# Kernel tuning notes

Hardware: AMD Instinct MI355X
Metric: run time of the kernel (lower is better)

The kernel has to match this reference:

```python
import jax, jax.numpy as jnp
import numpy as np

B, T, I, H, O = 256, 512, 64, 256, 16
THRESH = 1.0

def _xavier(key, fan_out, fan_in):
    bound = float(np.sqrt(6.0 / (fan_in + fan_out)))
    return jax.random.uniform(key, (fan_out, fan_in), jnp.float32, -bound, bound)

def setup_inputs() -> dict:
    key = jax.random.key(0)
    k = jax.random.split(key, 4)
    return {
        "x": jax.random.normal(k[0], (B, T, I), jnp.float32),
        "W_i2h": _xavier(k[1], H, I),
        "b_i2h": jnp.zeros((H,), jnp.float32),
        "W_h2h": 0.001 * jax.random.normal(k[2], (H, H), jnp.float32),  # trunc_normal std=0.001 approx
        "b_h2h": jnp.zeros((H,), jnp.float32),
        "W_out": _xavier(k[3], O, H),
        "b_out": jnp.zeros((O,), jnp.float32),
        "hidden_init": jnp.zeros((1, H), jnp.float32),
    }

def reference(x, W_i2h, b_i2h, W_h2h, b_h2h, W_out, b_out, hidden_init):
    # Precompute input projection for all timesteps in one GEMM: [B,T,H]
    xi = jnp.einsum('bti,hi->bth', x, W_i2h) + b_i2h
    h0 = jnp.tile(hidden_init, (x.shape[0], 1))  # [B,H]

    def step(h, xt):
        pre = h + xt + h @ W_h2h.T + b_h2h
        a = jnp.minimum(jax.nn.relu(pre), jnp.float32(THRESH))
        return a, a

    hidden, rnn_out_t = jax.lax.scan(step, h0, jnp.swapaxes(xi, 0, 1))  # [T,B,H]
    rnn_out = jnp.swapaxes(rnn_out_t, 0, 1)  # [B,T,H]
    output = rnn_out @ W_out.T + b_out  # [B,T,O]
    return (output, hidden, rnn_out)
```

## Files before the change

kernel.cpp:

```cpp
#include <hip/hip_runtime.h>

#define NB 256
#define NT 512
#define NI 64
#define NH 256
#define NO 16

typedef __attribute__((ext_vector_type(8))) short short8;
typedef __attribute__((ext_vector_type(8))) __bf16 bf16x8;
typedef __attribute__((ext_vector_type(2))) float f32x2;
typedef __attribute__((ext_vector_type(4))) float f32x4;
typedef __attribute__((ext_vector_type(4))) int int4v;
typedef __attribute__((ext_vector_type(8))) int int8v;

#define XI_STRIDE 260

__device__ __forceinline__ unsigned short f2bf(float f) {
  unsigned u = __builtin_bit_cast(unsigned, f);
  u += 0x7fffu + ((u >> 16) & 1u);
  return (unsigned short)(u >> 16);
}

__device__ __forceinline__ f32x4 mfma16(short8 a, short8 b, f32x4 c) {
  return __builtin_amdgcn_mfma_f32_16x16x32_bf16(
      __builtin_bit_cast(bf16x8, a), __builtin_bit_cast(bf16x8, b), c, 0, 0, 0);
}

__device__ __forceinline__ f32x4 mfma_fp8(int8v a, int8v b, f32x4 c) {
  return __builtin_amdgcn_mfma_scale_f32_16x16x128_f8f6f4(
      a, b, c, 0, 0, 0, 0x7f7f7f7f, 0, 0x7f7f7f7f);
}

__device__ __forceinline__ short8 pack8v(f32x4 lo, f32x4 hi) {
  short8 r;
#pragma unroll
  for (int i = 0; i < 4; ++i) {
    r[i]     = (short)f2bf(lo[i]);
    r[i + 4] = (short)f2bf(hi[i]);
  }
  return r;
}

__device__ __forceinline__ short8 pack8(const float* __restrict__ p) {
  return pack8v(*reinterpret_cast<const f32x4*>(p),
                *reinterpret_cast<const f32x4*>(p + 4));
}

__device__ __forceinline__ void step_barrier() {
  asm volatile("s_waitcnt lgkmcnt(0)" ::: "memory");
  __builtin_amdgcn_s_barrier();
  asm volatile("" ::: "memory");
}

__global__ __launch_bounds__(512, 2)
void rnn_fused(const float* __restrict__ x,  const float* __restrict__ Wi,
               const float* __restrict__ bi, const float* __restrict__ Wh,
               const float* __restrict__ bh, const float* __restrict__ Wo,
               const float* __restrict__ bo, const float* __restrict__ h0,
               float* __restrict__ dout)
{
  const int b   = blockIdx.x;
  const int tid = threadIdx.x;
  const int w   = tid >> 6;
  const int l   = tid & 63;
  const int lg  = l >> 4;
  const int ll  = l & 15;

  __shared__ __align__(16) unsigned char  hq8[2][256];
  __shared__ __align__(16) unsigned short rnnwin[16 * NH];
  __shared__ __align__(16) float          xi_t[16 * XI_STRIDE];

  float* outp = dout;
  float* hidp = dout + (size_t)NB * NT * NO;
  float* rnnp = hidp + (size_t)NB * NH;

  const f32x4 cz = {0.f, 0.f, 0.f, 0.f};

  int8v wq8[2][2];
  float dq[2];
#pragma unroll
  for (int jt = 0; jt < 2; ++jt) {
    const int j = w * 32 + 2 * ll + jt;
    const float* wr = Wh + (size_t)j * NH;
    float m = 0.f;
#pragma unroll
    for (int kc = 0; kc < 2; ++kc)
#pragma unroll
      for (int q8 = 0; q8 < 8; ++q8) {
        f32x4 v = *reinterpret_cast<const f32x4*>(wr + kc * 128 + lg * 32 + q8 * 4);
#pragma unroll
        for (int i = 0; i < 4; ++i) m = fmaxf(m, fabsf(v[i]));
      }
    m = fmaxf(m, __shfl_xor(m, 16));
    m = fmaxf(m, __shfl_xor(m, 32));
    const float s = (m > 0.f) ? 224.f / m : 0.f;
    dq[jt] = m * (1.f / 224.f);
#pragma unroll
    for (int kc = 0; kc < 2; ++kc) {
      int8v t8;
#pragma unroll
      for (int q8 = 0; q8 < 8; ++q8) {
        f32x4 v = *reinterpret_cast<const f32x4*>(wr + kc * 128 + lg * 32 + q8 * 4);
        int lo = __builtin_amdgcn_cvt_pk_fp8_f32(v[0] * s, v[1] * s, 0, false);
        t8[q8] = __builtin_amdgcn_cvt_pk_fp8_f32(v[2] * s, v[3] * s, lo, true);
      }
      wq8[jt][kc] = t8;
    }
  }

  short8 wif[2][2];
#pragma unroll
  for (int jt = 0; jt < 2; ++jt) {
    const int j = w * 32 + jt * 16 + ll;
#pragma unroll
    for (int kx = 0; kx < 2; ++kx)
      wif[jt][kx] = pack8(Wi + (size_t)j * NI + kx * 32 + lg * 8);
  }

  const int je = w * 32 + 2 * ll;
  const float breg0 = bi[je]     + bh[je];
  const float breg1 = bi[je + 1] + bh[je + 1];
  const float bout = bo[ll];

  float h_reg0 = h0[je];
  float h_reg1 = h0[je + 1];

  if (tid < 128) {
    int v = __builtin_amdgcn_cvt_pk_fp8_f32(h0[2 * tid], h0[2 * tid + 1], 0, false);
    *(unsigned short*)&hq8[0][2 * tid] = (unsigned short)v;
  }

  const float* xrow = x + (size_t)b * NT * NI + (size_t)ll * NI + lg * 8;
  f32x4 xpre[4];
  xpre[0] = *reinterpret_cast<const f32x4*>(xrow);
  xpre[1] = *reinterpret_cast<const f32x4*>(xrow + 4);
  xpre[2] = *reinterpret_cast<const f32x4*>(xrow + 32);
  xpre[3] = *reinterpret_cast<const f32x4*>(xrow + 36);

  __syncthreads();

  auto outproj = [&](int tbase) {
    f32x4 oacc = cz;
#pragma unroll
    for (int kt = 0; kt < 8; ++kt) {
      short8 wo = pack8(Wo + (size_t)ll * NH + kt * 32 + lg * 8);
      const char* ap = (const char*)rnnwin + ll * 512 +
                       ((kt * 64 + lg * 16) ^ (ll << 4));
      short8 af = *reinterpret_cast<const short8*>(ap);
      oacc = mfma16(af, wo, oacc);
    }
#pragma unroll
    for (int r = 0; r < 4; ++r) {
      const int tp = lg * 4 + r;
      outp[((size_t)b * NT + tbase - 16 + tp) * NO + ll] = oacc[r] + bout;
    }
  };

#pragma unroll 1
  for (int t0 = 0; t0 < NT; t0 += 16) {
    if (t0 > 0 && w == 0) outproj(t0);
    {
      short8 xf0 = pack8v(xpre[0], xpre[1]);
      short8 xf1 = pack8v(xpre[2], xpre[3]);
#pragma unroll
      for (int jt = 0; jt < 2; ++jt) {
        f32x4 acc = mfma16(xf0, wif[jt][0], cz);
        acc = mfma16(xf1, wif[jt][1], acc);
        const int j = w * 32 + jt * 16 + ll;
#pragma unroll
        for (int r = 0; r < 4; ++r)
          xi_t[(lg * 4 + r) * XI_STRIDE + j] = acc[r];
      }
    }
    if (t0 + 16 < NT) {
      const float* xp = x + (size_t)b * NT * NI + (size_t)(t0 + 16 + ll) * NI + lg * 8;
      xpre[0] = *reinterpret_cast<const f32x4*>(xp);
      xpre[1] = *reinterpret_cast<const f32x4*>(xp + 4);
      xpre[2] = *reinterpret_cast<const f32x4*>(xp + 32);
      xpre[3] = *reinterpret_cast<const f32x4*>(xp + 36);
    }
    step_barrier();

#define STEP(TT)                                                               \
    {                                                                          \
      const int t    = (TT);                                                   \
      const int trow = t & 15;                                                 \
      const int p    = t & 1;                                                  \
      const unsigned char* hb = hq8[p];                                        \
      int8v A0, A1;                                                            \
      *(int4v*)&A0       = *(const int4v*)(hb + lg * 32);                      \
      *((int4v*)&A0 + 1) = *(const int4v*)(hb + lg * 32 + 16);                 \
      *(int4v*)&A1       = *(const int4v*)(hb + 128 + lg * 32);                \
      *((int4v*)&A1 + 1) = *(const int4v*)(hb + 128 + lg * 32 + 16);           \
      f32x2 xi2 = *(const f32x2*)&xi_t[trow * XI_STRIDE + je];                 \
      const float hxi0 = h_reg0 + xi2[0] + breg0;                              \
      const float hxi1 = h_reg1 + xi2[1] + breg1;                              \
      f32x4 acc0 = mfma_fp8(A0, wq8[0][0], cz);                                \
      f32x4 acc1 = mfma_fp8(A0, wq8[1][0], cz);                                \
      acc0 = mfma_fp8(A1, wq8[0][1], acc0);                                    \
      acc1 = mfma_fp8(A1, wq8[1][1], acc1);                                    \
      const float a0 = fminf(fmaxf(fmaf(acc0[0], dq[0], hxi0), 0.f), 1.f);     \
      const float a1 = fminf(fmaxf(fmaf(acc1[0], dq[1], hxi1), 0.f), 1.f);     \
      h_reg0 = a0; h_reg1 = a1;                                                \
      if (lg == 0) {                                                           \
        int hv = __builtin_amdgcn_cvt_pk_fp8_f32(a0, a1, 0, false);            \
        *(unsigned short*)&hq8[p ^ 1][je] = (unsigned short)hv;                \
        *(unsigned*)((char*)rnnwin + trow * 512 +                              \
                     ((4 * (w * 16 + ll)) ^ (trow << 4))) =                    \
            (unsigned)f2bf(a0) | ((unsigned)f2bf(a1) << 16);                   \
        f32x2 o2; o2[0] = a0; o2[1] = a1;                                      \
        *(f32x2*)(rnnp + ((size_t)b * NT + t) * NH + je) = o2;                 \
      }                                                                        \
      step_barrier();                                                          \
    }

#pragma unroll 1
    for (int tt = 0; tt < 16; tt += 2) {
      STEP(t0 + tt)
      STEP(t0 + tt + 1)
    }
#undef STEP
  }

  if (w == 0) outproj(NT);
  if (lg == 0) {
    f32x2 h2; h2[0] = h_reg0; h2[1] = h_reg1;
    *(f32x2*)(hidp + (size_t)b * NH + je) = h2;
  }
}

extern "C" void kernel_launch(void* const* d_in, const int* in_sizes, int n_in,
                              void* d_out, int out_size, void* d_ws, size_t ws_size,
                              hipStream_t stream) {
  const float* x  = (const float*)d_in[0];
  const float* Wi = (const float*)d_in[1];
  const float* bi = (const float*)d_in[2];
  const float* Wh = (const float*)d_in[3];
  const float* bh = (const float*)d_in[4];
  const float* Wo = (const float*)d_in[5];
  const float* bo = (const float*)d_in[6];
  const float* h0 = (const float*)d_in[7];
  rnn_fused<<<dim3(NB), dim3(512), 0, stream>>>(x, Wi, bi, Wh, bh, Wo, bo, h0,
                                                (float*)d_out);
}
```

Before: 206.0 us.

## Split recurrence across 16 waves, one hidden unit per lane

Doubles the block to 1024 threads so each wave owns 16 hidden units and runs two fp8 MFMAs per step instead of four. This shortens the serial per-step critical path. The input projection, with the bias folded in, is stored per hidden unit so each lane loads its 16 timesteps into registers once per window. The output-projection duty rotates across waves. In exchange, each step's barrier now synchronises twice as many waves, and register pressure per thread rises under the new launch bounds.

```diff
diff --git a/kernel.cpp b/kernel.cpp
--- a/kernel.cpp
+++ b/kernel.cpp
@@ -8,12 +8,9 @@
 
 typedef __attribute__((ext_vector_type(8))) short short8;
 typedef __attribute__((ext_vector_type(8))) __bf16 bf16x8;
-typedef __attribute__((ext_vector_type(2))) float f32x2;
 typedef __attribute__((ext_vector_type(4))) float f32x4;
 typedef __attribute__((ext_vector_type(4))) int int4v;
 typedef __attribute__((ext_vector_type(8))) int int8v;
-
-#define XI_STRIDE 260
 
 __device__ __forceinline__ unsigned short f2bf(float f) {
   unsigned u = __builtin_bit_cast(unsigned, f);
@@ -52,7 +49,7 @@
   asm volatile("" ::: "memory");
 }
 
-__global__ __launch_bounds__(512, 2)
+__global__ __launch_bounds__(1024, 4)
 void rnn_fused(const float* __restrict__ x,  const float* __restrict__ Wi,
                const float* __restrict__ bi, const float* __restrict__ Wh,
                const float* __restrict__ bh, const float* __restrict__ Wo,
@@ -68,7 +65,7 @@
 
   __shared__ __align__(16) unsigned char  hq8[2][256];
   __shared__ __align__(16) unsigned short rnnwin[16 * NH];
-  __shared__ __align__(16) float          xi_t[16 * XI_STRIDE];
+  __shared__ __align__(16) float          xi_lds[NH * 20];
 
   float* outp = dout;
   float* hidp = dout + (size_t)NB * NT * NO;
@@ -76,11 +73,12 @@
 
   const f32x4 cz = {0.f, 0.f, 0.f, 0.f};
 
-  int8v wq8[2][2];
-  float dq[2];
-#pragma unroll
-  for (int jt = 0; jt < 2; ++jt) {
-    const int j = w * 32 + 2 * ll + jt;
+  const int j   = w * 16 + ll;
+  const int j20 = j * 20;
+
+  int8v wq8[2];
+  float dq;
+  {
     const float* wr = Wh + (size_t)j * NH;
     float m = 0.f;
 #pragma unroll
@@ -94,7 +92,7 @@
     m = fmaxf(m, __shfl_xor(m, 16));
     m = fmaxf(m, __shfl_xor(m, 32));
     const float s = (m > 0.f) ? 224.f / m : 0.f;
-    dq[jt] = m * (1.f / 224.f);
+    dq = m * (1.f / 224.f);
 #pragma unroll
     for (int kc = 0; kc < 2; ++kc) {
       int8v t8;
@@ -104,26 +102,18 @@
         int lo = __builtin_amdgcn_cvt_pk_fp8_f32(v[0] * s, v[1] * s, 0, false);
         t8[q8] = __builtin_amdgcn_cvt_pk_fp8_f32(v[2] * s, v[3] * s, lo, true);
       }
-      wq8[jt][kc] = t8;
-    }
-  }
-
-  short8 wif[2][2];
-#pragma unroll
-  for (int jt = 0; jt < 2; ++jt) {
-    const int j = w * 32 + jt * 16 + ll;
-#pragma unroll
-    for (int kx = 0; kx < 2; ++kx)
-      wif[jt][kx] = pack8(Wi + (size_t)j * NI + kx * 32 + lg * 8);
-  }
-
-  const int je = w * 32 + 2 * ll;
-  const float breg0 = bi[je]     + bh[je];
-  const float breg1 = bi[je + 1] + bh[je + 1];
+      wq8[kc] = t8;
+    }
+  }
+
+  short8 wif[2];
+#pragma unroll
+  for (int kx = 0; kx < 2; ++kx)
+    wif[kx] = pack8(Wi + (size_t)j * NI + kx * 32 + lg * 8);
+
+  const float breg = bi[j] + bh[j];
   const float bout = bo[ll];
-
-  float h_reg0 = h0[je];
-  float h_reg1 = h0[je + 1];
+  float h_reg = h0[j];
 
   if (tid < 128) {
     int v = __builtin_amdgcn_cvt_pk_fp8_f32(h0[2 * tid], h0[2 * tid + 1], 0, false);
@@ -156,21 +146,46 @@
     }
   };
 
+#define STEP(TT, XIV)                                                          \
+  {                                                                            \
+    const int t    = (TT);                                                     \
+    const int trow = t & 15;                                                   \
+    const int p    = t & 1;                                                    \
+    const unsigned char* hb = hq8[p];                                          \
+    int8v A0, A1;                                                              \
+    *(int4v*)&A0       = *(const int4v*)(hb + lg * 32);                        \
+    *((int4v*)&A0 + 1) = *(const int4v*)(hb + lg * 32 + 16);                   \
+    *(int4v*)&A1       = *(const int4v*)(hb + 128 + lg * 32);                  \
+    *((int4v*)&A1 + 1) = *(const int4v*)(hb + 128 + lg * 32 + 16);             \
+    const float hx = h_reg + (XIV);                   \
+    f32x4 acc0 = mfma_fp8(A0, wq8[0], cz);                                     \
+    f32x4 acc1 = mfma_fp8(A1, wq8[1], cz);                                     \
+    const float a = fminf(fmaxf(fmaf(acc0[0] + acc1[0], dq, hx), 0.f), 1.f);   \
+    h_reg = a;                                                                 \
+    if (lg == 0) {                                                             \
+      int hv = __builtin_amdgcn_cvt_pk_fp8_f32(a, a, 0, false);                \
+      hq8[p ^ 1][j] = (unsigned char)hv;                                       \
+      unsigned bfp;                                                            \
+      asm("v_cvt_pk_bf16_f32 %0, %1, %2" : "=v"(bfp) : "v"(a), "v"(a));        \
+      *(unsigned short*)((char*)rnnwin + trow * 512 +                          \
+                         ((2 * j) ^ (trow << 4))) = (unsigned short)bfp;       \
+      rnnp[((size_t)b * NT + t) * NH + j] = a;                                 \
+    }                                                                          \
+    step_barrier();                                                            \
+  }
+
 #pragma unroll 1
   for (int t0 = 0; t0 < NT; t0 += 16) {
-    if (t0 > 0 && w == 0) outproj(t0);
+    if (t0 > 0 && w == (((t0 >> 4) - 1) & 15)) outproj(t0);
     {
       short8 xf0 = pack8v(xpre[0], xpre[1]);
       short8 xf1 = pack8v(xpre[2], xpre[3]);
-#pragma unroll
-      for (int jt = 0; jt < 2; ++jt) {
-        f32x4 acc = mfma16(xf0, wif[jt][0], cz);
-        acc = mfma16(xf1, wif[jt][1], acc);
-        const int j = w * 32 + jt * 16 + ll;
-#pragma unroll
-        for (int r = 0; r < 4; ++r)
-          xi_t[(lg * 4 + r) * XI_STRIDE + j] = acc[r];
-      }
+      f32x4 acc = mfma16(xf0, wif[0], cz);
+      acc = mfma16(xf1, wif[1], acc);
+      f32x4 xo;
+#pragma unroll
+      for (int r = 0; r < 4; ++r) xo[r] = acc[r] + breg;
+      *(f32x4*)&xi_lds[j20 + lg * 4] = xo;
     }
     if (t0 + 16 < NT) {
       const float* xp = x + (size_t)b * NT * NI + (size_t)(t0 + 16 + ll) * NI + lg * 8;
@@ -181,52 +196,24 @@
     }
     step_barrier();
 
-#define STEP(TT)                                                               \
-    {                                                                          \
-      const int t    = (TT);                                                   \
-      const int trow = t & 15;                                                 \
-      const int p    = t & 1;                                                  \
-      const unsigned char* hb = hq8[p];                                        \
-      int8v A0, A1;                                                            \
-      *(int4v*)&A0       = *(const int4v*)(hb + lg * 32);                      \
-      *((int4v*)&A0 + 1) = *(const int4v*)(hb + lg * 32 + 16);                 \
-      *(int4v*)&A1       = *(const int4v*)(hb + 128 + lg * 32);                \
-      *((int4v*)&A1 + 1) = *(const int4v*)(hb + 128 + lg * 32 + 16);           \
-      f32x2 xi2 = *(const f32x2*)&xi_t[trow * XI_STRIDE + je];                 \
-      const float hxi0 = h_reg0 + xi2[0] + breg0;                              \
-      const float hxi1 = h_reg1 + xi2[1] + breg1;                              \
-      f32x4 acc0 = mfma_fp8(A0, wq8[0][0], cz);                                \
-      f32x4 acc1 = mfma_fp8(A0, wq8[1][0], cz);                                \
-      acc0 = mfma_fp8(A1, wq8[0][1], acc0);                                    \
-      acc1 = mfma_fp8(A1, wq8[1][1], acc1);                                    \
-      const float a0 = fminf(fmaxf(fmaf(acc0[0], dq[0], hxi0), 0.f), 1.f);     \
-      const float a1 = fminf(fmaxf(fmaf(acc1[0], dq[1], hxi1), 0.f), 1.f);     \
-      h_reg0 = a0; h_reg1 = a1;                                                \
-      if (lg == 0) {                                                           \
-        int hv = __builtin_amdgcn_cvt_pk_fp8_f32(a0, a1, 0, false);            \
-        *(unsigned short*)&hq8[p ^ 1][je] = (unsigned short)hv;                \
-        *(unsigned*)((char*)rnnwin + trow * 512 +                              \
-                     ((4 * (w * 16 + ll)) ^ (trow << 4))) =                    \
-            (unsigned)f2bf(a0) | ((unsigned)f2bf(a1) << 16);                   \
-        f32x2 o2; o2[0] = a0; o2[1] = a1;                                      \
-        *(f32x2*)(rnnp + ((size_t)b * NT + t) * NH + je) = o2;                 \
-      }                                                                        \
-      step_barrier();                                                          \
-    }
-
-#pragma unroll 1
-    for (int tt = 0; tt < 16; tt += 2) {
-      STEP(t0 + tt)
-      STEP(t0 + tt + 1)
-    }
+    f32x4 xq0 = *(const f32x4*)&xi_lds[j20];
+    f32x4 xq1 = *(const f32x4*)&xi_lds[j20 + 4];
+    f32x4 xq2 = *(const f32x4*)&xi_lds[j20 + 8];
+    f32x4 xq3 = *(const f32x4*)&xi_lds[j20 + 12];
+
+    STEP(t0 + 0,  xq0[0]) STEP(t0 + 1,  xq0[1])
+    STEP(t0 + 2,  xq0[2]) STEP(t0 + 3,  xq0[3])
+    STEP(t0 + 4,  xq1[0]) STEP(t0 + 5,  xq1[1])
+    STEP(t0 + 6,  xq1[2]) STEP(t0 + 7,  xq1[3])
+    STEP(t0 + 8,  xq2[0]) STEP(t0 + 9,  xq2[1])
+    STEP(t0 + 10, xq2[2]) STEP(t0 + 11, xq2[3])
+    STEP(t0 + 12, xq3[0]) STEP(t0 + 13, xq3[1])
+    STEP(t0 + 14, xq3[2]) STEP(t0 + 15, xq3[3])
+  }
 #undef STEP
-  }
-
-  if (w == 0) outproj(NT);
-  if (lg == 0) {
-    f32x2 h2; h2[0] = h_reg0; h2[1] = h_reg1;
-    *(f32x2*)(hidp + (size_t)b * NH + je) = h2;
-  }
+
+  if (w == 15) outproj(NT);
+  if (lg == 0) hidp[(size_t)b * NH + j] = h_reg;
 }
 
 extern "C" void kernel_launch(void* const* d_in, const int* in_sizes, int n_in,
@@ -240,6 +227,6 @@
   const float* Wo = (const float*)d_in[5];
   const float* bo = (const float*)d_in[6];
   const float* h0 = (const float*)d_in[7];
-  rnn_fused<<<dim3(NB), dim3(512), 0, stream>>>(x, Wi, bi, Wh, bh, Wo, bo, h0,
-                                                (float*)d_out);
-}
+  rnn_fused<<<dim3(NB), dim3(1024), 0, stream>>>(x, Wi, bi, Wh, bh, Wo, bo, h0,
+                                                 (float*)d_out);
+}
```

Measured after the change: 249.7 us. 21.2% more time.

## Prefetch xi into registers per chunk, split MFMA chains, rotate outproj wave

Applied to the files above, without the earlier changes.

The xi tile is stored transposed (hidden-major) with the bias folded in. Each thread loads its 16 timesteps of xi into registers once per 16-step chunk, so the per-step LDS read and bias add leave the serial recurrence. The two dependent fp8 MFMAs per output become four independent MFMAs summed afterwards, and the clamp uses med3, both to shorten the per-step latency chain. The output-projection work now rotates across waves instead of always landing on wave 0, at the cost of more registers from full unrolling.

```diff
diff --git a/kernel.cpp b/kernel.cpp
--- a/kernel.cpp
+++ b/kernel.cpp
@@ -12,8 +12,6 @@
 typedef __attribute__((ext_vector_type(4))) float f32x4;
 typedef __attribute__((ext_vector_type(4))) int int4v;
 typedef __attribute__((ext_vector_type(8))) int int8v;
-
-#define XI_STRIDE 260
 
 __device__ __forceinline__ unsigned short f2bf(float f) {
   unsigned u = __builtin_bit_cast(unsigned, f);
@@ -68,7 +66,7 @@
 
   __shared__ __align__(16) unsigned char  hq8[2][256];
   __shared__ __align__(16) unsigned short rnnwin[16 * NH];
-  __shared__ __align__(16) float          xi_t[16 * XI_STRIDE];
+  __shared__ __align__(16) float          xi_t[NH * 20];
 
   float* outp = dout;
   float* hidp = dout + (size_t)NB * NT * NO;
@@ -109,17 +107,17 @@
   }
 
   short8 wif[2][2];
+  float bregW[2];
 #pragma unroll
   for (int jt = 0; jt < 2; ++jt) {
     const int j = w * 32 + jt * 16 + ll;
 #pragma unroll
     for (int kx = 0; kx < 2; ++kx)
       wif[jt][kx] = pack8(Wi + (size_t)j * NI + kx * 32 + lg * 8);
+    bregW[jt] = bi[j] + bh[j];
   }
 
   const int je = w * 32 + 2 * ll;
-  const float breg0 = bi[je]     + bh[je];
-  const float breg1 = bi[je + 1] + bh[je + 1];
   const float bout = bo[ll];
 
   float h_reg0 = h0[je];
@@ -156,9 +154,43 @@
     }
   };
 
+#define STEP(TT, XIV0, XIV1)                                                   \
+  {                                                                            \
+    const int t    = (TT);                                                     \
+    const int trow = t & 15;                                                   \
+    const int p    = t & 1;                                                    \
+    const unsigned char* hb = hq8[p];                                          \
+    int8v A0, A1;                                                              \
+    *(int4v*)&A0       = *(const int4v*)(hb + lg * 32);                        \
+    *((int4v*)&A0 + 1) = *(const int4v*)(hb + lg * 32 + 16);                   \
+    *(int4v*)&A1       = *(const int4v*)(hb + 128 + lg * 32);                  \
+    *((int4v*)&A1 + 1) = *(const int4v*)(hb + 128 + lg * 32 + 16);             \
+    const float hx0 = h_reg0 + (XIV0);                    \
+    const float hx1 = h_reg1 + (XIV1);                                         \
+    f32x4 a00 = mfma_fp8(A0, wq8[0][0], cz);                                   \
+    f32x4 a10 = mfma_fp8(A0, wq8[1][0], cz);                                   \
+    f32x4 a01 = mfma_fp8(A1, wq8[0][1], cz);                                   \
+    f32x4 a11 = mfma_fp8(A1, wq8[1][1], cz);                                   \
+    const float s0 = a00[0] + a01[0];                                          \
+    const float s1 = a10[0] + a11[0];                                          \
+    const float a0 = __builtin_amdgcn_fmed3f(fmaf(s0, dq[0], hx0), 0.f, 1.f);  \
+    const float a1 = __builtin_amdgcn_fmed3f(fmaf(s1, dq[1], hx1), 0.f, 1.f);  \
+    h_reg0 = a0; h_reg1 = a1;                                                  \
+    if (lg == 0) {                                                             \
+      int hv = __builtin_amdgcn_cvt_pk_fp8_f32(a0, a1, 0, false);              \
+      *(unsigned short*)&hq8[p ^ 1][je] = (unsigned short)hv;                  \
+      *(unsigned*)((char*)rnnwin + trow * 512 +                                \
+                   ((4 * (w * 16 + ll)) ^ (trow << 4))) =                      \
+          (unsigned)f2bf(a0) | ((unsigned)f2bf(a1) << 16);                     \
+      f32x2 o2; o2[0] = a0; o2[1] = a1;                                        \
+      *(f32x2*)(rnnp + ((size_t)b * NT + t) * NH + je) = o2;                   \
+    }                                                                          \
+    step_barrier();                                                            \
+  }
+
 #pragma unroll 1
   for (int t0 = 0; t0 < NT; t0 += 16) {
-    if (t0 > 0 && w == 0) outproj(t0);
+    if (t0 > 0 && w == (((t0 >> 4) - 1) & 7)) outproj(t0);
     {
       short8 xf0 = pack8v(xpre[0], xpre[1]);
       short8 xf1 = pack8v(xpre[2], xpre[3]);
@@ -167,9 +199,10 @@
         f32x4 acc = mfma16(xf0, wif[jt][0], cz);
         acc = mfma16(xf1, wif[jt][1], acc);
         const int j = w * 32 + jt * 16 + ll;
-#pragma unroll
-        for (int r = 0; r < 4; ++r)
-          xi_t[(lg * 4 + r) * XI_STRIDE + j] = acc[r];
+        f32x4 xo;
+#pragma unroll
+        for (int r = 0; r < 4; ++r) xo[r] = acc[r] + bregW[jt];
+        *(f32x4*)&xi_t[j * 20 + lg * 4] = xo;
       }
     }
     if (t0 + 16 < NT) {
@@ -181,48 +214,25 @@
     }
     step_barrier();
 
-#define STEP(TT)                                                               \
-    {                                                                          \
-      const int t    = (TT);                                                   \
-      const int trow = t & 15;                                                 \
-      const int p    = t & 1;                                                  \
-      const unsigned char* hb = hq8[p];                                        \
-      int8v A0, A1;                                                            \
-      *(int4v*)&A0       = *(const int4v*)(hb + lg * 32);                      \
-      *((int4v*)&A0 + 1) = *(const int4v*)(hb + lg * 32 + 16);                 \
-      *(int4v*)&A1       = *(const int4v*)(hb + 128 + lg * 32);                \
-      *((int4v*)&A1 + 1) = *(const int4v*)(hb + 128 + lg * 32 + 16);           \
-      f32x2 xi2 = *(const f32x2*)&xi_t[trow * XI_STRIDE + je];                 \
-      const float hxi0 = h_reg0 + xi2[0] + breg0;                              \
-      const float hxi1 = h_reg1 + xi2[1] + breg1;                              \
-      f32x4 acc0 = mfma_fp8(A0, wq8[0][0], cz);                                \
-      f32x4 acc1 = mfma_fp8(A0, wq8[1][0], cz);                                \
-      acc0 = mfma_fp8(A1, wq8[0][1], acc0);                                    \
-      acc1 = mfma_fp8(A1, wq8[1][1], acc1);                                    \
-      const float a0 = fminf(fmaxf(fmaf(acc0[0], dq[0], hxi0), 0.f), 1.f);     \
-      const float a1 = fminf(fmaxf(fmaf(acc1[0], dq[1], hxi1), 0.f), 1.f);     \
-      h_reg0 = a0; h_reg1 = a1;                                                \
-      if (lg == 0) {                                                           \
-        int hv = __builtin_amdgcn_cvt_pk_fp8_f32(a0, a1, 0, false);            \
-        *(unsigned short*)&hq8[p ^ 1][je] = (unsigned short)hv;                \
-        *(unsigned*)((char*)rnnwin + trow * 512 +                              \
-                     ((4 * (w * 16 + ll)) ^ (trow << 4))) =                    \
-            (unsigned)f2bf(a0) | ((unsigned)f2bf(a1) << 16);                   \
-        f32x2 o2; o2[0] = a0; o2[1] = a1;                                      \
-        *(f32x2*)(rnnp + ((size_t)b * NT + t) * NH + je) = o2;                 \
-      }                                                                        \
-      step_barrier();                                                          \
-    }
-
-#pragma unroll 1
-    for (int tt = 0; tt < 16; tt += 2) {
-      STEP(t0 + tt)
-      STEP(t0 + tt + 1)
-    }
+    f32x4 xqe[4], xqo[4];
+#pragma unroll
+    for (int q = 0; q < 4; ++q) {
+      xqe[q] = *(const f32x4*)&xi_t[je * 20 + q * 4];
+      xqo[q] = *(const f32x4*)&xi_t[(je + 1) * 20 + q * 4];
+    }
+
+    STEP(t0 + 0,  xqe[0][0], xqo[0][0]) STEP(t0 + 1,  xqe[0][1], xqo[0][1])
+    STEP(t0 + 2,  xqe[0][2], xqo[0][2]) STEP(t0 + 3,  xqe[0][3], xqo[0][3])
+    STEP(t0 + 4,  xqe[1][0], xqo[1][0]) STEP(t0 + 5,  xqe[1][1], xqo[1][1])
+    STEP(t0 + 6,  xqe[1][2], xqo[1][2]) STEP(t0 + 7,  xqe[1][3], xqo[1][3])
+    STEP(t0 + 8,  xqe[2][0], xqo[2][0]) STEP(t0 + 9,  xqe[2][1], xqo[2][1])
+    STEP(t0 + 10, xqe[2][2], xqo[2][2]) STEP(t0 + 11, xqe[2][3], xqo[2][3])
+    STEP(t0 + 12, xqe[3][0], xqo[3][0]) STEP(t0 + 13, xqe[3][1], xqo[3][1])
+    STEP(t0 + 14, xqe[3][2], xqo[3][2]) STEP(t0 + 15, xqe[3][3], xqo[3][3])
+  }
 #undef STEP
-  }
-
-  if (w == 0) outproj(NT);
+
+  if (w == 7) outproj(NT);
   if (lg == 0) {
     f32x2 h2; h2[0] = h_reg0; h2[1] = h_reg1;
     *(f32x2*)(hidp + (size_t)b * NH + je) = h2;
```

Measured after the change: 192.6 us. -6.5%, faster.
